# Performance work log

Hardware: AMD Instinct MI355X
Metric: run time of the kernel (lower is better)

The kernel has to match this reference:

```python
import jax, jax.numpy as jnp
import numpy as np

B, T, C = 4, 4096, 1024
H = 16          # n_head
LS = 256        # local block size (block-causal window)
EPS = 1e-6


def rmsnorm(x, w):
    # matches RMSNorm: x * rsqrt(mean(x^2) + eps) * weight, computed in fp32
    xf = x.astype(jnp.float32)
    y = xf * jax.lax.rsqrt(jnp.mean(xf * xf, axis=-1, keepdims=True) + EPS)
    return y.astype(x.dtype) * w


def setup_inputs() -> dict:
    key = jax.random.key(0)
    k1, k2, k3 = jax.random.split(key, 3)
    x = jax.random.normal(k1, (B, T, C), dtype=jnp.float32)
    w_qkv = jax.random.normal(k2, (C, 3 * C), dtype=jnp.float32) * (1.0 / np.sqrt(C))
    ln_w = jnp.ones((C,), dtype=jnp.float32)
    w_proj = jax.random.normal(k3, (C, C), dtype=jnp.float32) * (1.0 / np.sqrt(C))
    return {"x": x, "w_qkv": w_qkv, "ln_w": ln_w, "w_proj": w_proj}


def reference(x, w_qkv, ln_w, w_proj):
    Bx, Tx, Cx = x.shape
    ng = Tx // LS                      # number of causal blocks
    hd = Cx // H                       # head dim
    # group tokens into blocks: [B, ng, ls, C]
    xg = x.reshape(Bx, ng, LS, Cx)
    qkv = jnp.einsum('bglc,cd->bgld', xg, w_qkv)
    q, k, v = jnp.split(qkv, 3, axis=-1)
    # fused QK RMSNorm over full embed dim (before head split), shared weight
    q = rmsnorm(q, ln_w)
    k = rmsnorm(k, ln_w)
    # split heads: [B, ng, H, ls, hd]
    q = q.reshape(Bx, ng, LS, H, hd).transpose(0, 1, 3, 2, 4)
    k = k.reshape(Bx, ng, LS, H, hd).transpose(0, 1, 3, 2, 4)
    v = v.reshape(Bx, ng, LS, H, hd).transpose(0, 1, 3, 2, 4)
    scale = 1.0 / np.sqrt(hd)          # muP=False
    att = jnp.einsum('bghqd,bghkd->bghqk', q, k) * scale
    causal = jnp.tril(jnp.ones((LS, LS), dtype=bool))
    att = jnp.where(causal, att, -jnp.finfo(att.dtype).max)
    att = jax.nn.softmax(att, axis=-1)
    y = jnp.einsum('bghqk,bghkd->bghqd', att, v)
    # merge heads and blocks back: [B, T, C]
    y = y.transpose(0, 1, 3, 2, 4).reshape(Bx, Tx, Cx)
    return jnp.einsum('btc,cd->btd', y, w_proj)
```

## Files before the change

kernel.cpp:

```cpp
#include <hip/hip_runtime.h>

typedef __attribute__((ext_vector_type(4))) float f32x4;
typedef __attribute__((ext_vector_type(8))) short bf16x8;
typedef __attribute__((ext_vector_type(4))) unsigned short u16x4;
typedef __attribute__((ext_vector_type(8))) unsigned short u16x8;
typedef unsigned short u16;
typedef unsigned int u32;

#define M_  16384
#define C_  1024
#define N1_ 3072
#define PSZ ((size_t)M_ * 64 * 16 / 16 * 4 / 4)

__device__ __forceinline__ float bf2f(u16 u) {
  union { u32 i; float f; } v; v.i = ((u32)u) << 16; return v.f;
}
__device__ __forceinline__ u16 f2bf(float f) {
  union { float f; u32 i; } v; v.f = f;
  u32 r = v.i + 0x7fffu + ((v.i >> 16) & 1u);
  return (u16)(r >> 16);
}

__device__ __forceinline__ void gload16(const void* g, void* l) {
  __builtin_amdgcn_global_load_lds(
      (const __attribute__((address_space(1))) u32*)g,
      (__attribute__((address_space(3))) u32*)l, 16, 0, 0);
}

__global__ __launch_bounds__(256) void cast_f32_bf16(const float* __restrict__ in,
                                                     u16* __restrict__ out) {
  size_t i = (size_t)blockIdx.x * 256 + threadIdx.x;
  f32x4 v = ((const f32x4*)in)[i];
  u16x4 o = { f2bf(v[0]), f2bf(v[1]), f2bf(v[2]), f2bf(v[3]) };
  ((u16x4*)out)[i] = o;
}

__global__ __launch_bounds__(256) void transpose_cast(const float* __restrict__ in,
                                                      u16* __restrict__ out, int K, int N) {
  __shared__ u16 tile[64][65];
  const int n0 = blockIdx.x * 64, k0 = blockIdx.y * 64;
  const int tid = threadIdx.x;
  const int nn = tid & 63, kk = tid >> 6;
#pragma unroll
  for (int r = 0; r < 16; ++r)
    tile[kk * 16 + r][nn] = f2bf(in[(size_t)(k0 + kk * 16 + r) * N + n0 + nn]);
  __syncthreads();
  const int kc = tid & 15, nl = tid >> 4;
#pragma unroll
  for (int p = 0; p < 4; ++p) {
    const int n = p * 16 + nl;
    u16x4 v = { tile[kc * 4 + 0][n], tile[kc * 4 + 1][n],
                tile[kc * 4 + 2][n], tile[kc * 4 + 3][n] };
    *(u16x4*)(out + (size_t)(n0 + n) * K + k0 + kc * 4) = v;
  }
}

__device__ __forceinline__ void store16(float* dst, f32x4 v0, f32x4 v1, f32x4 v2, f32x4 v3) {
  ((f32x4*)dst)[0] = v0; ((f32x4*)dst)[1] = v1; ((f32x4*)dst)[2] = v2; ((f32x4*)dst)[3] = v3;
}
__device__ __forceinline__ void store16(u16* dst, f32x4 v0, f32x4 v1, f32x4 v2, f32x4 v3) {
  u16x8 o0 = { f2bf(v0[0]), f2bf(v0[1]), f2bf(v0[2]), f2bf(v0[3]),
               f2bf(v1[0]), f2bf(v1[1]), f2bf(v1[2]), f2bf(v1[3]) };
  u16x8 o1 = { f2bf(v2[0]), f2bf(v2[1]), f2bf(v2[2]), f2bf(v2[3]),
               f2bf(v3[0]), f2bf(v3[1]), f2bf(v3[2]), f2bf(v3[3]) };
  *(u16x8*)dst = o0; *(u16x8*)(dst + 8) = o1;
}

template <typename OUT>
__global__ __launch_bounds__(512, 2) void gemm256(const u16* __restrict__ A,
                                                  const u16* __restrict__ BT,
                                                  OUT* __restrict__ C,
                                                  int M, int N, int ntn,
                                                  float* __restrict__ ssq,
                                                  float* __restrict__ ssk) {
  constexpr int KC = 1024;
  __shared__ __align__(16) u16 sA0[256 * 64], sA1[256 * 64];
  __shared__ __align__(16) u16 sB0[256 * 64], sB1[256 * 64];
  __shared__ float ssred[4][256];
  const int tid = threadIdx.x, lane = tid & 63, w = tid >> 6;
  const int wm = w >> 2, wn = w & 3;

  int bid = blockIdx.x;
  const int cpx = gridDim.x >> 3;
  bid = (bid & 7) * cpx + (bid >> 3);
  const int tm = (bid / ntn) << 8, tn = (bid % ntn) << 8;

  const u16* srcA[4]; const u16* srcB[4]; int ldsOff[4];
#pragma unroll
  for (int l = 0; l < 4; ++l) {
    const int g = l * 512 + tid;
    const int row = g >> 3, c = g & 7;
    srcA[l] = A + (size_t)(tm + row) * KC + ((c ^ (row & 7)) << 3);
    srcB[l] = BT + (size_t)(tn + row) * KC + ((c ^ (row & 7)) << 3);
    ldsOff[l] = g << 4;
  }

#define STAGE(sa, sb, kt) do { const int _k0 = (kt) << 6;                      \
    _Pragma("unroll") for (int _l = 0; _l < 4; ++_l) {                         \
      gload16(srcA[_l] + _k0, (char*)(sa) + ldsOff[_l]);                       \
      gload16(srcB[_l] + _k0, (char*)(sb) + ldsOff[_l]); } } while (0)

  const int swz = (lane & 7) << 4;
  const int r16 = lane & 15;
  const int kb = (lane >> 4) << 4;
#define LDA_(sa, fm, ks) (*(const bf16x8*)((const char*)(sa) + \
    (wm * 128 + (fm) * 16 + r16) * 128 + ((((ks) << 6) | kb) ^ swz)))
#define LDB_(sb, fn, ks) (*(const bf16x8*)((const char*)(sb) + \
    (wn * 64 + (fn) * 16 + r16) * 128 + ((((ks) << 6) | kb) ^ swz)))

  f32x4 acc[8][4];
#pragma unroll
  for (int i = 0; i < 8; ++i)
#pragma unroll
    for (int j = 0; j < 4; ++j) acc[i][j] = (f32x4){0.f, 0.f, 0.f, 0.f};

#define MM(i, j, a_, b_) acc[i][j] = __builtin_amdgcn_mfma_f32_16x16x32_bf16(a_, b_, acc[i][j], 0, 0, 0)

#define KTILE(sa, sb, ...) do {                                                \
  bf16x8 ka[4][2], kb0[2][2], kb1[2][2];                                       \
  _Pragma("unroll") for (int fm = 0; fm < 4; ++fm) {                           \
    ka[fm][0] = LDA_(sa, fm, 0); ka[fm][1] = LDA_(sa, fm, 1); }                \
  _Pragma("unroll") for (int fn = 0; fn < 2; ++fn) {                           \
    kb0[fn][0] = LDB_(sb, fn, 0); kb0[fn][1] = LDB_(sb, fn, 1); }              \
  __builtin_amdgcn_s_barrier();                                                \
  __builtin_amdgcn_s_setprio(1);                                               \
  _Pragma("unroll") for (int fm = 0; fm < 4; ++fm)                             \
    _Pragma("unroll") for (int fn = 0; fn < 2; ++fn) {                         \
      MM(fm, fn, ka[fm][0], kb0[fn][0]); MM(fm, fn, ka[fm][1], kb0[fn][1]); }  \
  __builtin_amdgcn_s_setprio(0);                                               \
  __builtin_amdgcn_s_barrier();                                                \
  _Pragma("unroll") for (int fn = 0; fn < 2; ++fn) {                           \
    kb1[fn][0] = LDB_(sb, 2 + fn, 0); kb1[fn][1] = LDB_(sb, 2 + fn, 1); }      \
  __builtin_amdgcn_s_barrier();                                                \
  __builtin_amdgcn_s_setprio(1);                                               \
  _Pragma("unroll") for (int fm = 0; fm < 4; ++fm)                             \
    _Pragma("unroll") for (int fn = 0; fn < 2; ++fn) {                         \
      MM(fm, 2 + fn, ka[fm][0], kb1[fn][0]); MM(fm, 2 + fn, ka[fm][1], kb1[fn][1]); } \
  __builtin_amdgcn_s_setprio(0);                                               \
  __builtin_amdgcn_s_barrier();                                                \
  _Pragma("unroll") for (int fm = 0; fm < 4; ++fm) {                           \
    ka[fm][0] = LDA_(sa, 4 + fm, 0); ka[fm][1] = LDA_(sa, 4 + fm, 1); }        \
  __builtin_amdgcn_s_barrier();                                                \
  __builtin_amdgcn_s_setprio(1);                                               \
  _Pragma("unroll") for (int fm = 0; fm < 4; ++fm)                             \
    _Pragma("unroll") for (int fn = 0; fn < 2; ++fn) {                         \
      MM(4 + fm, 2 + fn, ka[fm][0], kb1[fn][0]); MM(4 + fm, 2 + fn, ka[fm][1], kb1[fn][1]); } \
  __builtin_amdgcn_s_setprio(0);                                               \
  __builtin_amdgcn_s_barrier();                                                \
  __builtin_amdgcn_sched_barrier(0);                                           \
  __VA_ARGS__;                                                                 \
  __builtin_amdgcn_s_setprio(1);                                               \
  _Pragma("unroll") for (int fm = 0; fm < 4; ++fm)                             \
    _Pragma("unroll") for (int fn = 0; fn < 2; ++fn) {                         \
      MM(4 + fm, fn, ka[fm][0], kb0[fn][0]); MM(4 + fm, fn, ka[fm][1], kb0[fn][1]); } \
  __builtin_amdgcn_s_setprio(0);                                               \
} while (0)

#define TILE_ENTRY(vm) do { __builtin_amdgcn_sched_barrier(0);                 \
    asm volatile("s_waitcnt vmcnt(" #vm ")");                                  \
    __builtin_amdgcn_sched_barrier(0);                                         \
    __builtin_amdgcn_s_barrier();                                              \
    __builtin_amdgcn_sched_barrier(0); } while (0)

  STAGE(sA0, sB0, 0);
  STAGE(sA1, sB1, 1);

#pragma unroll 1
  for (int i = 0; i < 7; ++i) {
    TILE_ENTRY(8);
    KTILE(sA0, sB0, STAGE(sA0, sB0, 2 * i + 2));
    TILE_ENTRY(8);
    KTILE(sA1, sB1, STAGE(sA1, sB1, 2 * i + 3));
  }
  TILE_ENTRY(8);
  KTILE(sA0, sB0, (void)0);
  TILE_ENTRY(0);
  KTILE(sA1, sB1, (void)0);

  __syncthreads();

  const int part = tn >> 10;
  const int cp = tn & 1023;
  const int bg = tm >> 8;
  const int hh = (cp >> 6) + wn;
  if constexpr (sizeof(OUT) == 2) {
    if (part < 2) {
#pragma unroll
      for (int fm = 0; fm < 8; ++fm)
#pragma unroll
        for (int r = 0; r < 4; ++r) {
          float s = acc[fm][0][r] * acc[fm][0][r] + acc[fm][1][r] * acc[fm][1][r]
                  + acc[fm][2][r] * acc[fm][2][r] + acc[fm][3][r] * acc[fm][3][r];
          s += __shfl_xor(s, 1, 64); s += __shfl_xor(s, 2, 64);
          s += __shfl_xor(s, 4, 64); s += __shfl_xor(s, 8, 64);
          if (r16 == 0) ssred[wn][wm * 128 + fm * 16 + (lane >> 4) * 4 + r] = s;
        }
      __syncthreads();
      if (tid < 256) {
        float s = ssred[0][tid] + ssred[1][tid] + ssred[2][tid] + ssred[3][tid];
        (part == 0 ? ssq : ssk)[(size_t)(tm + tid) * 4 + (cp >> 8)] = s;
      }
    }
  }

  u16* eb = (w == 0) ? sA0 : (w == 1) ? sA0 + 8192 : (w == 2) ? sA1 : (w == 3) ? sA1 + 8192
          : (w == 4) ? sB0 : (w == 5) ? sB0 + 8192 : (w == 6) ? sB1 : sB1 + 8192;
  float* fb = (float*)eb;
  const int erow = lane >> 2, eseg = lane & 3;
  OUT* dstb;
  if constexpr (sizeof(OUT) == 2)
    dstb = C + (size_t)part * ((size_t)M_ * C_) + ((size_t)(bg * 16 + hh) * 256) * 64;
  else
    dstb = C + (size_t)(tm) * N + tn + wn * 64;
#pragma unroll
  for (int fm = 0; fm < 8; ++fm) {
#pragma unroll
    for (int fn = 0; fn < 4; ++fn)
#pragma unroll
      for (int r = 0; r < 4; ++r)
        fb[((lane >> 4) * 4 + r) * 68 + fn * 16 + (lane & 15)] = acc[fm][fn][r];
    asm volatile("s_waitcnt lgkmcnt(0)" ::: "memory");
    const float* src = &fb[erow * 68 + eseg * 16];
    f32x4 v0 = ((const f32x4*)src)[0], v1 = ((const f32x4*)src)[1];
    f32x4 v2 = ((const f32x4*)src)[2], v3 = ((const f32x4*)src)[3];
    OUT* dst;
    if constexpr (sizeof(OUT) == 2)
      dst = dstb + (size_t)(wm * 128 + fm * 16 + erow) * 64 + eseg * 16;
    else
      dst = dstb + (size_t)(wm * 128 + fm * 16 + erow) * N + eseg * 16;
    store16(dst, v0, v1, v2, v3);
  }
#undef STAGE
#undef LDA_
#undef LDB_
#undef MM
#undef KTILE
#undef TILE_ENTRY
}

__global__ __launch_bounds__(256, 2) void attn_kernel(const u16* __restrict__ qkvblk,
                                                      const float* __restrict__ ssq,
                                                      const float* __restrict__ ssk,
                                                      const float* __restrict__ lnw,
                                                      u16* __restrict__ y) {
  const int bid = blockIdx.x;
  const int h = bid & 15;
  const int bg = bid >> 4;
  const size_t rowbase = (size_t)bg * 256;
  const u16* Qb = qkvblk + ((size_t)(bg * 16 + h) * 256) * 64;
  const u16* Kb = Qb + (size_t)M_ * C_;
  const u16* Vb = Qb + 2 * (size_t)M_ * C_;

  __shared__ __align__(16) u16 Vt[64 * 256];
  __shared__ __align__(16) u16 Ps[4][16 * 256];
  __shared__ float kscl[256];

  const int tid = threadIdx.x;
  const int lane = tid & 63;
  const int w = tid >> 6;
  const int g = lane >> 4;
  const int qi = lane & 15;

  {
    const int r = tid;
    const u16* vr = Vb + (size_t)r * 64;
#pragma unroll
    for (int j = 0; j < 8; ++j) {
      bf16x8 vv = *(const bf16x8*)(vr + j * 8);
#pragma unroll
      for (int e = 0; e < 8; ++e) {
        int d = j * 8 + e;
        *(u16*)((char*)Vt + d * 512 + ((2 * r) ^ ((d & 7) << 4))) = (u16)vv[e];
      }
    }
    f32x4 kp = ((const f32x4*)ssk)[rowbase + r];
    kscl[r] = rsqrtf((kp[0] + kp[1] + kp[2] + kp[3]) * (1.0f / 1024.0f) + 1e-6f);
  }
  float lnq0[8], lnq1[8];
#pragma unroll
  for (int e = 0; e < 8; ++e) {
    float a = lnw[h * 64 + g * 8 + e];
    float b = lnw[h * 64 + 32 + g * 8 + e];
    lnq0[e] = a * a; lnq1[e] = b * b;
  }
  __syncthreads();

  char* pb = (char*)Ps[w];
  const int swq = (qi & 7) << 4;

#pragma unroll 1
  for (int j = 0; j < 4; ++j) {
    const int qt = ((j >> 1) << 3) + ((j & 1) ? (7 - w) : w);
    const int q = qt * 16 + qi;

    f32x4 qv = ((const f32x4*)ssq)[rowbase + q];
    const float qsc = rsqrtf((qv[0] + qv[1] + qv[2] + qv[3]) * (1.0f / 1024.0f) + 1e-6f);
    const u16* qrow = Qb + (size_t)q * 64 + g * 8;
    bf16x8 q0 = *(const bf16x8*)(qrow);
    bf16x8 q1 = *(const bf16x8*)(qrow + 32);
#pragma unroll
    for (int e = 0; e < 8; ++e) {
      q0[e] = (short)f2bf(bf2f((u16)q0[e]) * qsc * lnq0[e]);
      q1[e] = (short)f2bf(bf2f((u16)q1[e]) * qsc * lnq1[e]);
    }

    f32x4 s[16];
#pragma unroll
    for (int n = 0; n < 16; ++n) {
      if (n <= qt) {
        const u16* krow = Kb + (size_t)(n * 16 + qi) * 64 + g * 8;
        bf16x8 ka0 = *(const bf16x8*)(krow);
        bf16x8 ka1 = *(const bf16x8*)(krow + 32);
        f32x4 a = {0.f, 0.f, 0.f, 0.f};
        a = __builtin_amdgcn_mfma_f32_16x16x32_bf16(ka0, q0, a, 0, 0, 0);
        a = __builtin_amdgcn_mfma_f32_16x16x32_bf16(ka1, q1, a, 0, 0, 0);
        s[n] = a;
      }
    }

    float m = -3e38f;
#pragma unroll
    for (int n = 0; n < 16; ++n) if (n <= qt) {
      f32x4 k4 = *(const f32x4*)&kscl[n * 16 + g * 4];
#pragma unroll
      for (int r = 0; r < 4; ++r) {
        const int k_abs = n * 16 + g * 4 + r;
        float v = s[n][r] * 0.125f * k4[r];
        v = (k_abs <= q) ? v : -3e38f;
        s[n][r] = v;
        m = fmaxf(m, v);
      }
    }
    m = fmaxf(m, __shfl_xor(m, 16, 64));
    m = fmaxf(m, __shfl_xor(m, 32, 64));

    float sum = 0.f;
#pragma unroll
    for (int n = 0; n < 16; ++n) if (n <= qt) {
#pragma unroll
      for (int r = 0; r < 4; ++r) {
        float p = __expf(s[n][r] - m);
        s[n][r] = p;
        sum += p;
      }
    }
    sum += __shfl_xor(sum, 16, 64);
    sum += __shfl_xor(sum, 32, 64);

#pragma unroll
    for (int n = 0; n < 16; ++n) if (n <= qt) {
      u16x4 pk = { f2bf(s[n][0]), f2bf(s[n][1]), f2bf(s[n][2]), f2bf(s[n][3]) };
      *(u16x4*)(pb + qi * 512 + ((n * 32 + g * 8) ^ swq)) = pk;
    }
    if (!(qt & 1)) {
      u16x4 z = {0, 0, 0, 0};
      *(u16x4*)(pb + qi * 512 + (((qt + 1) * 32 + g * 8) ^ swq)) = z;
    }

    f32x4 yacc[4];
#pragma unroll
    for (int dn = 0; dn < 4; ++dn) yacc[dn] = (f32x4){0.f, 0.f, 0.f, 0.f};
    const int nkf = qt / 2 + 1;
#pragma unroll
    for (int kf = 0; kf < 8; ++kf) if (kf < nkf) {
      bf16x8 pa = *(const bf16x8*)(pb + qi * 512 + ((kf * 64 + g * 16) ^ swq));
#pragma unroll
      for (int dn = 0; dn < 4; ++dn) {
        const int d = dn * 16 + qi;
        bf16x8 vb = *(const bf16x8*)((const char*)Vt + d * 512 + ((kf * 64 + g * 16) ^ swq));
        yacc[dn] = __builtin_amdgcn_mfma_f32_16x16x32_bf16(pa, vb, yacc[dn], 0, 0, 0);
      }
    }

#pragma unroll
    for (int r = 0; r < 4; ++r) {
      const float inv = 1.0f / __shfl(sum, g * 4 + r, 64);
      const size_t trow = rowbase + (size_t)qt * 16 + g * 4 + r;
      u16* yrow = y + trow * C_ + h * 64 + qi;
#pragma unroll
      for (int dn = 0; dn < 4; ++dn) yrow[dn * 16] = f2bf(yacc[dn][r] * inv);
    }
  }
}

extern "C" void kernel_launch(void* const* d_in, const int* in_sizes, int n_in,
                              void* d_out, int out_size, void* d_ws, size_t ws_size,
                              hipStream_t stream) {
  const float* x      = (const float*)d_in[0];
  const float* w_qkv  = (const float*)d_in[1];
  const float* ln_w   = (const float*)d_in[2];
  const float* w_proj = (const float*)d_in[3];
  float* out = (float*)d_out;

  u16* xb     = (u16*)d_ws;
  u16* wqkvT  = xb + (size_t)M_ * C_;
  u16* wprojT = wqkvT + (size_t)N1_ * C_;
  u16* qkvblk = wprojT + (size_t)C_ * C_;
  u16* yb     = qkvblk + 3 * (size_t)M_ * C_;
  float* ssq  = (float*)(yb + (size_t)M_ * C_);
  float* ssk  = ssq + (size_t)M_ * 4;

  cast_f32_bf16<<<(M_ * C_) / 1024, 256, 0, stream>>>(x, xb);
  transpose_cast<<<dim3(N1_ / 64, C_ / 64), 256, 0, stream>>>(w_qkv, wqkvT, C_, N1_);
  transpose_cast<<<dim3(C_ / 64, C_ / 64), 256, 0, stream>>>(w_proj, wprojT, C_, C_);

  gemm256<u16><<<(M_ / 256) * (N1_ / 256), 512, 0, stream>>>(xb, wqkvT, qkvblk, M_, N1_, N1_ / 256, ssq, ssk);
  attn_kernel<<<64 * 16, 256, 0, stream>>>(qkvblk, ssq, ssk, ln_w, yb);
  gemm256<float><<<(M_ / 256) * (C_ / 256), 512, 0, stream>>>(yb, wprojT, out, M_, C_, C_ / 256, nullptr, nullptr);
}
```

Baseline: 258.5 us.

## Store attention output head-blocked, halve P buffer, raise attention occupancy

The attention kernel now writes its output in a head-blocked layout (per block-group and head, 256x64 contiguous), staged through LDS so each lane issues 16-byte coalesced stores instead of scattered 2-byte stores. The projection GEMM gets a template flag that reads its A operand from this layout, with a K step of 16384 elements per tile. The P scratch buffer is halved by doing the PV product in two passes, and the LN weights move to shared memory. Together these cut shared memory and registers so launch bounds can rise to 4 blocks per CU.

```diff
diff --git a/kernel.cpp b/kernel.cpp
--- a/kernel.cpp
+++ b/kernel.cpp
@@ -10,7 +10,6 @@
 #define M_  16384
 #define C_  1024
 #define N1_ 3072
-#define PSZ ((size_t)M_ * 64 * 16 / 16 * 4 / 4)
 
 __device__ __forceinline__ float bf2f(u16 u) {
   union { u32 i; float f; } v; v.i = ((u32)u) << 16; return v.f;
@@ -66,14 +65,15 @@
   *(u16x8*)dst = o0; *(u16x8*)(dst + 8) = o1;
 }
 
-template <typename OUT>
+template <typename OUT, bool AHB>
 __global__ __launch_bounds__(512, 2) void gemm256(const u16* __restrict__ A,
                                                   const u16* __restrict__ BT,
                                                   OUT* __restrict__ C,
                                                   int M, int N, int ntn,
                                                   float* __restrict__ ssq,
                                                   float* __restrict__ ssk) {
-  constexpr int KC = 1024;
+  constexpr int ARS   = AHB ? 64 : 1024;
+  constexpr int ASTEP = AHB ? 16384 : 64;
   __shared__ __align__(16) u16 sA0[256 * 64], sA1[256 * 64];
   __shared__ __align__(16) u16 sB0[256 * 64], sB1[256 * 64];
   __shared__ float ssred[4][256];
@@ -90,15 +90,15 @@
   for (int l = 0; l < 4; ++l) {
     const int g = l * 512 + tid;
     const int row = g >> 3, c = g & 7;
-    srcA[l] = A + (size_t)(tm + row) * KC + ((c ^ (row & 7)) << 3);
-    srcB[l] = BT + (size_t)(tn + row) * KC + ((c ^ (row & 7)) << 3);
+    srcA[l] = A + (size_t)tm * 1024 + (size_t)row * ARS + ((c ^ (row & 7)) << 3);
+    srcB[l] = BT + (size_t)(tn + row) * 1024 + ((c ^ (row & 7)) << 3);
     ldsOff[l] = g << 4;
   }
 
-#define STAGE(sa, sb, kt) do { const int _k0 = (kt) << 6;                      \
+#define STAGE(sa, sb, kt) do {                                                 \
     _Pragma("unroll") for (int _l = 0; _l < 4; ++_l) {                         \
-      gload16(srcA[_l] + _k0, (char*)(sa) + ldsOff[_l]);                       \
-      gload16(srcB[_l] + _k0, (char*)(sb) + ldsOff[_l]); } } while (0)
+      gload16(srcA[_l] + (kt) * ASTEP, (char*)(sa) + ldsOff[_l]);              \
+      gload16(srcB[_l] + (kt) * 64, (char*)(sb) + ldsOff[_l]); } } while (0)
 
   const int swz = (lane & 7) << 4;
   const int r16 = lane & 15;
@@ -211,7 +211,7 @@
   if constexpr (sizeof(OUT) == 2)
     dstb = C + (size_t)part * ((size_t)M_ * C_) + ((size_t)(bg * 16 + hh) * 256) * 64;
   else
-    dstb = C + (size_t)(tm) * N + tn + wn * 64;
+    dstb = C + (size_t)tm * N + tn + wn * 64;
 #pragma unroll
   for (int fm = 0; fm < 8; ++fm) {
 #pragma unroll
@@ -238,7 +238,7 @@
 #undef TILE_ENTRY
 }
 
-__global__ __launch_bounds__(256, 2) void attn_kernel(const u16* __restrict__ qkvblk,
+__global__ __launch_bounds__(256, 4) void attn_kernel(const u16* __restrict__ qkvblk,
                                                       const float* __restrict__ ssq,
                                                       const float* __restrict__ ssk,
                                                       const float* __restrict__ lnw,
@@ -250,10 +250,12 @@
   const u16* Qb = qkvblk + ((size_t)(bg * 16 + h) * 256) * 64;
   const u16* Kb = Qb + (size_t)M_ * C_;
   const u16* Vb = Qb + 2 * (size_t)M_ * C_;
+  u16* Yb = y + ((size_t)(bg * 16 + h) * 256) * 64;
 
   __shared__ __align__(16) u16 Vt[64 * 256];
-  __shared__ __align__(16) u16 Ps[4][16 * 256];
+  __shared__ __align__(16) u16 Ps[4][16 * 128];
   __shared__ float kscl[256];
+  __shared__ float lnsq[64];
 
   const int tid = threadIdx.x;
   const int lane = tid & 63;
@@ -275,13 +277,7 @@
     }
     f32x4 kp = ((const f32x4*)ssk)[rowbase + r];
     kscl[r] = rsqrtf((kp[0] + kp[1] + kp[2] + kp[3]) * (1.0f / 1024.0f) + 1e-6f);
-  }
-  float lnq0[8], lnq1[8];
-#pragma unroll
-  for (int e = 0; e < 8; ++e) {
-    float a = lnw[h * 64 + g * 8 + e];
-    float b = lnw[h * 64 + 32 + g * 8 + e];
-    lnq0[e] = a * a; lnq1[e] = b * b;
+    if (tid < 64) { float a = lnw[h * 64 + tid]; lnsq[tid] = a * a; }
   }
   __syncthreads();
 
@@ -298,10 +294,16 @@
     const u16* qrow = Qb + (size_t)q * 64 + g * 8;
     bf16x8 q0 = *(const bf16x8*)(qrow);
     bf16x8 q1 = *(const bf16x8*)(qrow + 32);
-#pragma unroll
-    for (int e = 0; e < 8; ++e) {
-      q0[e] = (short)f2bf(bf2f((u16)q0[e]) * qsc * lnq0[e]);
-      q1[e] = (short)f2bf(bf2f((u16)q1[e]) * qsc * lnq1[e]);
+    {
+      f32x4 wa0 = *(const f32x4*)&lnsq[g * 8],      wa1 = *(const f32x4*)&lnsq[g * 8 + 4];
+      f32x4 wb0 = *(const f32x4*)&lnsq[32 + g * 8], wb1 = *(const f32x4*)&lnsq[32 + g * 8 + 4];
+#pragma unroll
+      for (int e = 0; e < 4; ++e) {
+        q0[e]     = (short)f2bf(bf2f((u16)q0[e]) * qsc * wa0[e]);
+        q0[4 + e] = (short)f2bf(bf2f((u16)q0[4 + e]) * qsc * wa1[e]);
+        q1[e]     = (short)f2bf(bf2f((u16)q1[e]) * qsc * wb0[e]);
+        q1[4 + e] = (short)f2bf(bf2f((u16)q1[4 + e]) * qsc * wb1[e]);
+      }
     }
 
     f32x4 s[16];
@@ -347,23 +349,23 @@
     sum += __shfl_xor(sum, 16, 64);
     sum += __shfl_xor(sum, 32, 64);
 
-#pragma unroll
-    for (int n = 0; n < 16; ++n) if (n <= qt) {
-      u16x4 pk = { f2bf(s[n][0]), f2bf(s[n][1]), f2bf(s[n][2]), f2bf(s[n][3]) };
-      *(u16x4*)(pb + qi * 512 + ((n * 32 + g * 8) ^ swq)) = pk;
-    }
-    if (!(qt & 1)) {
-      u16x4 z = {0, 0, 0, 0};
-      *(u16x4*)(pb + qi * 512 + (((qt + 1) * 32 + g * 8) ^ swq)) = z;
-    }
-
     f32x4 yacc[4];
 #pragma unroll
     for (int dn = 0; dn < 4; ++dn) yacc[dn] = (f32x4){0.f, 0.f, 0.f, 0.f};
     const int nkf = qt / 2 + 1;
-#pragma unroll
-    for (int kf = 0; kf < 8; ++kf) if (kf < nkf) {
-      bf16x8 pa = *(const bf16x8*)(pb + qi * 512 + ((kf * 64 + g * 16) ^ swq));
+
+#pragma unroll
+    for (int n = 0; n < 8; ++n) if (n <= qt) {
+      u16x4 pk = { f2bf(s[n][0]), f2bf(s[n][1]), f2bf(s[n][2]), f2bf(s[n][3]) };
+      *(u16x4*)(pb + qi * 256 + ((n * 32 + g * 8) ^ swq)) = pk;
+    }
+    if (!(qt & 1) && qt < 7) {
+      u16x4 z = {0, 0, 0, 0};
+      *(u16x4*)(pb + qi * 256 + (((qt + 1) * 32 + g * 8) ^ swq)) = z;
+    }
+#pragma unroll
+    for (int kf = 0; kf < 4; ++kf) if (kf < nkf) {
+      bf16x8 pa = *(const bf16x8*)(pb + qi * 256 + ((kf * 64 + g * 16) ^ swq));
 #pragma unroll
       for (int dn = 0; dn < 4; ++dn) {
         const int d = dn * 16 + qi;
@@ -372,13 +374,42 @@
       }
     }
 
+    if (qt >= 8) {
+#pragma unroll
+      for (int n = 8; n < 16; ++n) if (n <= qt) {
+        u16x4 pk = { f2bf(s[n][0]), f2bf(s[n][1]), f2bf(s[n][2]), f2bf(s[n][3]) };
+        *(u16x4*)(pb + qi * 256 + (((n - 8) * 32 + g * 8) ^ swq)) = pk;
+      }
+      if (!(qt & 1)) {
+        u16x4 z = {0, 0, 0, 0};
+        *(u16x4*)(pb + qi * 256 + (((qt - 7) * 32 + g * 8) ^ swq)) = z;
+      }
+#pragma unroll
+      for (int kf = 4; kf < 8; ++kf) if (kf < nkf) {
+        bf16x8 pa = *(const bf16x8*)(pb + qi * 256 + (((kf - 4) * 64 + g * 16) ^ swq));
+#pragma unroll
+        for (int dn = 0; dn < 4; ++dn) {
+          const int d = dn * 16 + qi;
+          bf16x8 vb = *(const bf16x8*)((const char*)Vt + d * 512 + ((kf * 64 + g * 16) ^ swq));
+          yacc[dn] = __builtin_amdgcn_mfma_f32_16x16x32_bf16(pa, vb, yacc[dn], 0, 0, 0);
+        }
+      }
+    }
+
 #pragma unroll
     for (int r = 0; r < 4; ++r) {
       const float inv = 1.0f / __shfl(sum, g * 4 + r, 64);
-      const size_t trow = rowbase + (size_t)qt * 16 + g * 4 + r;
-      u16* yrow = y + trow * C_ + h * 64 + qi;
-#pragma unroll
-      for (int dn = 0; dn < 4; ++dn) yrow[dn * 16] = f2bf(yacc[dn][r] * inv);
+      const int row = g * 4 + r;
+#pragma unroll
+      for (int dn = 0; dn < 4; ++dn)
+        *(u16*)(pb + row * 128 + ((dn * 32 + qi * 2) ^ ((row & 7) << 4))) =
+            f2bf(yacc[dn][r] * inv);
+    }
+    const int rrow = lane >> 2, seg = lane & 3;
+#pragma unroll
+    for (int h2 = 0; h2 < 2; ++h2) {
+      u16x8 v = *(const u16x8*)(pb + rrow * 128 + ((seg * 32 + h2 * 16) ^ ((rrow & 7) << 4)));
+      *(u16x8*)(Yb + (size_t)(qt * 16 + rrow) * 64 + seg * 16 + h2 * 8) = v;
     }
   }
 }
@@ -404,7 +435,9 @@
   transpose_cast<<<dim3(N1_ / 64, C_ / 64), 256, 0, stream>>>(w_qkv, wqkvT, C_, N1_);
   transpose_cast<<<dim3(C_ / 64, C_ / 64), 256, 0, stream>>>(w_proj, wprojT, C_, C_);
 
-  gemm256<u16><<<(M_ / 256) * (N1_ / 256), 512, 0, stream>>>(xb, wqkvT, qkvblk, M_, N1_, N1_ / 256, ssq, ssk);
+  gemm256<u16, false><<<(M_ / 256) * (N1_ / 256), 512, 0, stream>>>(
+      xb, wqkvT, qkvblk, M_, N1_, N1_ / 256, ssq, ssk);
   attn_kernel<<<64 * 16, 256, 0, stream>>>(qkvblk, ssq, ssk, ln_w, yb);
-  gemm256<float><<<(M_ / 256) * (C_ / 256), 512, 0, stream>>>(yb, wprojT, out, M_, C_, C_ / 256, nullptr, nullptr);
-}
+  gemm256<float, true><<<(M_ / 256) * (C_ / 256), 512, 0, stream>>>(
+      yb, wprojT, out, M_, C_, C_ / 256, nullptr, nullptr);
+}
```

After: 314.5 us. 1.22x slower.
